# Optimization experiments

Hardware: AMD Instinct MI355X
Metric: run time of the kernel (lower is better)

## Reference

```python
import jax, jax.numpy as jnp
import numpy as np

TEMPERATURE = 0.07


def setup_inputs() -> dict:
    key = jax.random.key(0)
    k1, k2 = jax.random.split(key)
    B, D = 8192, 1024
    emb1 = jax.random.normal(k1, (B, D), dtype=jnp.float32)
    emb2 = jax.random.normal(k2, (B, D), dtype=jnp.float32)
    return {"emb1": emb1, "emb2": emb2}


def reference(emb1, emb2):
    B = emb1.shape[0]
    # [B, B] similarity logits scaled by temperature
    logits = jnp.matmul(emb1, emb2.T) / TEMPERATURE
    # SigLIP-style contrastive loss: diagonal entries are positives,
    # off-diagonal entries are negatives.
    # positive: -logsigmoid(logits) on diag; negative: -logsigmoid(-logits) off-diag
    pos = -jax.nn.log_sigmoid(jnp.diagonal(logits))            # [B]
    neg = -jax.nn.log_sigmoid(-logits)                          # [B, B]
    # negative_mask zeroes the diagonal -> subtract diagonal contribution
    neg_sum = neg.sum() - jnp.sum(jnp.diagonal(neg))
    loss = (pos.sum() + neg_sum) / B
    return loss
```

## Files before the change

kernel.cpp:

```cpp
#include <hip/hip_runtime.h>


#define B_DIM 8192
#define K_DIM 1024
#define BT 128
#define BKB 128
#define NT (K_DIM / BKB)
#define BRICK 16384
#define PANEL_BYTES (NT * BRICK)
#define BUFSZ 32768

typedef int i32x4 __attribute__((ext_vector_type(4)));
typedef int i32x8 __attribute__((ext_vector_type(8)));
typedef float f32x4 __attribute__((ext_vector_type(4)));

__device__ __forceinline__ void brick_store(const float* __restrict__ in,
                                            unsigned char* __restrict__ out,
                                            float scale, int i) {
  const int o = i * 16;
  const int b = o >> 14;
  const int p = b >> 3, t = b & 7;
  const int w = o & (BRICK - 1);
  const int fb = w >> 11;
  const int h = (w >> 10) & 1;
  const int kch = (w >> 8) & 3;
  const int lr = (w >> 4) & 15;
  const int row = p * 128 + fb * 16 + lr;
  const int kb = t * 128 + kch * 32 + h * 16;
  const float4* src = (const float4*)(in + (size_t)row * K_DIM + kb);
  float4 v0 = src[0], v1 = src[1], v2 = src[2], v3 = src[3];
  unsigned w0 = 0, w1 = 0, w2 = 0, w3 = 0;
  w0 = __builtin_amdgcn_cvt_pk_fp8_f32(v0.x * scale, v0.y * scale, w0, 0);
  w0 = __builtin_amdgcn_cvt_pk_fp8_f32(v0.z * scale, v0.w * scale, w0, 1);
  w1 = __builtin_amdgcn_cvt_pk_fp8_f32(v1.x * scale, v1.y * scale, w1, 0);
  w1 = __builtin_amdgcn_cvt_pk_fp8_f32(v1.z * scale, v1.w * scale, w1, 1);
  w2 = __builtin_amdgcn_cvt_pk_fp8_f32(v2.x * scale, v2.y * scale, w2, 0);
  w2 = __builtin_amdgcn_cvt_pk_fp8_f32(v2.z * scale, v2.w * scale, w2, 1);
  w3 = __builtin_amdgcn_cvt_pk_fp8_f32(v3.x * scale, v3.y * scale, w3, 0);
  w3 = __builtin_amdgcn_cvt_pk_fp8_f32(v3.z * scale, v3.w * scale, w3, 1);
  *(uint4*)(out + o) = make_uint4(w0, w1, w2, w3);
}

__global__ __launch_bounds__(256) void cvt_fused(
    const float* __restrict__ e1, const float* __restrict__ e2,
    unsigned char* __restrict__ A8, unsigned char* __restrict__ B8,
    int nbA, float scaleA) {
  const int blk = blockIdx.x;
  if (blk < nbA)
    brick_store(e1, A8, scaleA, blk * 256 + threadIdx.x);
  else
    brick_store(e2, B8, 1.0f, (blk - nbA) * 256 + threadIdx.x);
}

template <bool DIAG>
__device__ __forceinline__ float softplus_sum(const f32x4 (&acc)[4][4],
                                              int rbase, int cbase) {
  float lin = 0.f, cor = 0.f;
#pragma unroll
  for (int m = 0; m < 4; ++m) {
#pragma unroll
    for (int n = 0; n < 4; ++n) {
#pragma unroll
      for (int r = 0; r < 4; ++r) {
        float x = acc[m][n][r];
        if (DIAG) {
          int row = rbase + m * 16 + r;
          int col = cbase + n * 16;
          if (row == col) x = -x;
        }
        lin += fmaxf(x, 0.f);
        cor += __logf(1.f + __expf(-fabsf(x)));
      }
    }
  }
  return lin + cor;
}

#define STAGEA(SB, Q, TI)                                                     \
  __builtin_amdgcn_global_load_lds(                                           \
      (const __attribute__((address_space(1))) void*)(const void*)(           \
          srcA + (TI) * BRICK + (Q) * 1024),                                  \
      (__attribute__((address_space(3))) void*)(void*)(                       \
          lds + (SB) + dA + (Q) * 1024),                                      \
      16, 0, 0)
#define STAGEB(SB, Q, TI)                                                     \
  __builtin_amdgcn_global_load_lds(                                           \
      (const __attribute__((address_space(1))) void*)(const void*)(           \
          srcB + (TI) * BRICK + (Q) * 1024),                                  \
      (__attribute__((address_space(3))) void*)(void*)(                       \
          lds + (SB) + dB + (Q) * 1024),                                      \
      16, 0, 0)

#define LDA(OUT, RB, M)                                                       \
  {                                                                           \
    const unsigned char* _b = ldsL + ((RB) + ((wr * 4 + (M)) << 11));         \
    i32x4 _lo = *(const i32x4*)(_b);                                          \
    i32x4 _hi = *(const i32x4*)(_b + 1024);                                   \
    OUT = __builtin_shufflevector(_lo, _hi, 0, 1, 2, 3, 4, 5, 6, 7);          \
  }
#define LDB(OUT, RB, N)                                                       \
  {                                                                           \
    const unsigned char* _b = ldsL + ((RB) + 16384 + ((wc * 4 + (N)) << 11)); \
    i32x4 _lo = *(const i32x4*)(_b);                                          \
    i32x4 _hi = *(const i32x4*)(_b + 1024);                                   \
    OUT = __builtin_shufflevector(_lo, _hi, 0, 1, 2, 3, 4, 5, 6, 7);          \
  }

#define MFMA(AF, BF, M, N)                                                    \
  acc[M][N] = __builtin_amdgcn_mfma_scale_f32_16x16x128_f8f6f4(               \
      AF, BF, acc[M][N], 0, 0, 0, 127, 0, 127)

__global__ __launch_bounds__(256, 2) void siglip_gemm(
    const unsigned char* __restrict__ A8,
    const unsigned char* __restrict__ B8,
    float* __restrict__ partials) {
  __shared__ unsigned char lds[2 * BUFSZ];
  __shared__ float wsum[4];

  const int tid = threadIdx.x;
  const int wave = tid >> 6;
  const int lane = tid & 63;
  const int wr = wave >> 1;
  const int wc = wave & 1;
  const int brow = blockIdx.y;
  const int bcol = blockIdx.x;

  f32x4 acc[4][4];
#pragma unroll
  for (int m = 0; m < 4; ++m)
#pragma unroll
    for (int n = 0; n < 4; ++n) acc[m][n] = f32x4{0.f, 0.f, 0.f, 0.f};

  const unsigned char* srcA =
      A8 + (size_t)brow * PANEL_BYTES + wave * 4096 + (lane << 4);
  const unsigned char* srcB =
      B8 + (size_t)bcol * PANEL_BYTES + wave * 4096 + (lane << 4);
  const int dA = wave * 4096;
  const int dB = 16384 + wave * 4096;
  const unsigned char* ldsL = lds + (lane << 4);

  STAGEA(0, 0, 0); STAGEA(0, 1, 0); STAGEA(0, 2, 0); STAGEA(0, 3, 0);
  STAGEB(0, 0, 0); STAGEB(0, 1, 0); STAGEB(0, 2, 0); STAGEB(0, 3, 0);
  asm volatile("s_waitcnt vmcnt(0)" ::: "memory");
  __builtin_amdgcn_s_barrier();
  __builtin_amdgcn_sched_barrier(0);

#pragma unroll
  for (int T = 0; T < NT; ++T) {
    const int rb = (T & 1) * BUFSZ;
    const int sb = rb ^ BUFSZ;

    if (T < NT - 1) {
      STAGEA(sb, 0, T + 1); STAGEA(sb, 1, T + 1);
      STAGEA(sb, 2, T + 1); STAGEA(sb, 3, T + 1);
      STAGEB(sb, 0, T + 1); STAGEB(sb, 1, T + 1);
      STAGEB(sb, 2, T + 1); STAGEB(sb, 3, T + 1);
    }

    i32x8 a0, a1, a2, a3, b0, b1, b2, b3;
    LDA(a0, rb, 0); LDB(b0, rb, 0); LDB(b1, rb, 1); LDB(b2, rb, 2);
    LDB(b3, rb, 3);
    LDA(a1, rb, 1); LDA(a2, rb, 2); LDA(a3, rb, 3);

    __builtin_amdgcn_s_setprio(1);
    MFMA(a0, b0, 0, 0); MFMA(a0, b1, 0, 1); MFMA(a0, b2, 0, 2); MFMA(a0, b3, 0, 3);
    MFMA(a1, b0, 1, 0); MFMA(a1, b1, 1, 1); MFMA(a1, b2, 1, 2); MFMA(a1, b3, 1, 3);
    MFMA(a2, b0, 2, 0); MFMA(a2, b1, 2, 1); MFMA(a2, b2, 2, 2); MFMA(a2, b3, 2, 3);
    MFMA(a3, b0, 3, 0); MFMA(a3, b1, 3, 1); MFMA(a3, b2, 3, 2); MFMA(a3, b3, 3, 3);
    __builtin_amdgcn_s_setprio(0);

    if (T < NT - 1) {
      asm volatile("s_waitcnt vmcnt(0)" ::: "memory");
      __builtin_amdgcn_s_barrier();
      __builtin_amdgcn_sched_barrier(0);
    }
  }

  const int rbase = brow * BT + wr * 64 + (lane >> 4) * 4;
  const int cbase = bcol * BT + wc * 64 + (lane & 15);
  float lsum;
  if (brow == bcol)
    lsum = softplus_sum<true>(acc, rbase, cbase);
  else
    lsum = softplus_sum<false>(acc, rbase, cbase);

#pragma unroll
  for (int off = 32; off > 0; off >>= 1) lsum += __shfl_down(lsum, off);
  __syncthreads();
  if (lane == 0) wsum[wave] = lsum;
  __syncthreads();
  if (tid == 0)
    partials[blockIdx.y * gridDim.x + blockIdx.x] =
        wsum[0] + wsum[1] + wsum[2] + wsum[3];
}

__global__ void reduce_kernel(const float* __restrict__ partials, int n,
                              float* __restrict__ out) {
  __shared__ float s[256];
  float v = 0.f;
  for (int i = threadIdx.x; i < n; i += 256) v += partials[i];
  s[threadIdx.x] = v;
  __syncthreads();
  for (int off = 128; off > 0; off >>= 1) {
    if ((int)threadIdx.x < off) s[threadIdx.x] += s[threadIdx.x + off];
    __syncthreads();
  }
  if (threadIdx.x == 0) out[0] = s[0] / (float)B_DIM;
}

extern "C" void kernel_launch(void* const* d_in, const int* in_sizes, int n_in,
                              void* d_out, int out_size, void* d_ws, size_t ws_size,
                              hipStream_t stream) {
  const float* emb1 = (const float*)d_in[0];
  const float* emb2 = (const float*)d_in[1];

  unsigned char* A8 = (unsigned char*)d_ws;
  unsigned char* B8 = A8 + (size_t)B_DIM * K_DIM;
  float* partials = (float*)(B8 + (size_t)B_DIM * K_DIM);

  const float INV_T = 1.0f / 0.07f;
  const int nbA = (B_DIM * K_DIM / 16) / 256;
  cvt_fused<<<2 * nbA, 256, 0, stream>>>(emb1, emb2, A8, B8, nbA, INV_T);

  dim3 grid(B_DIM / BT, B_DIM / BT);
  siglip_gemm<<<grid, 256, 0, stream>>>(A8, B8, partials);

  const int nparts = (B_DIM / BT) * (B_DIM / BT);
  reduce_kernel<<<1, 256, 0, stream>>>(partials, nparts, (float*)d_out);
}
```

Baseline: 115.6 us.

## Use 256x128 tiles with 8 waves and a triple-buffered LDS pipeline

```diff
diff --git a/kernel.cpp b/kernel.cpp
--- a/kernel.cpp
+++ b/kernel.cpp
@@ -3,12 +3,11 @@
 
 #define B_DIM 8192
 #define K_DIM 1024
-#define BT 128
 #define BKB 128
 #define NT (K_DIM / BKB)
 #define BRICK 16384
 #define PANEL_BYTES (NT * BRICK)
-#define BUFSZ 32768
+#define BUFSZ 49152
 
 typedef int i32x4 __attribute__((ext_vector_type(4)));
 typedef int i32x8 __attribute__((ext_vector_type(8)));
@@ -90,32 +89,67 @@
       (__attribute__((address_space(3))) void*)(void*)(                       \
           lds + (SB) + dB + (Q) * 1024),                                      \
       16, 0, 0)
+#define STAGE6(SB, TI)                                                        \
+  STAGEA(SB, 0, TI); STAGEA(SB, 1, TI); STAGEA(SB, 2, TI); STAGEA(SB, 3, TI); \
+  STAGEB(SB, 0, TI); STAGEB(SB, 1, TI)
 
 #define LDA(OUT, RB, M)                                                       \
   {                                                                           \
-    const unsigned char* _b = ldsL + ((RB) + ((wr * 4 + (M)) << 11));         \
+    const unsigned char* _b =                                                 \
+        ldsL + ((RB) + ((wr >> 1) * 16384) + (((wr & 1) * 4 + (M)) << 11));   \
     i32x4 _lo = *(const i32x4*)(_b);                                          \
     i32x4 _hi = *(const i32x4*)(_b + 1024);                                   \
     OUT = __builtin_shufflevector(_lo, _hi, 0, 1, 2, 3, 4, 5, 6, 7);          \
   }
 #define LDB(OUT, RB, N)                                                       \
   {                                                                           \
-    const unsigned char* _b = ldsL + ((RB) + 16384 + ((wc * 4 + (N)) << 11)); \
+    const unsigned char* _b = ldsL + ((RB) + 32768 + ((wc * 4 + (N)) << 11)); \
     i32x4 _lo = *(const i32x4*)(_b);                                          \
     i32x4 _hi = *(const i32x4*)(_b + 1024);                                   \
     OUT = __builtin_shufflevector(_lo, _hi, 0, 1, 2, 3, 4, 5, 6, 7);          \
   }
-
-#define MFMA(AF, BF, M, N)                                                    \
+#define READS(RB, FA, FB)                                                     \
+  LDA(FA[0], RB, 0); LDB(FB[0], RB, 0); LDB(FB[1], RB, 1);                    \
+  LDB(FB[2], RB, 2); LDB(FB[3], RB, 3);                                       \
+  LDA(FA[1], RB, 1); LDA(FA[2], RB, 2); LDA(FA[3], RB, 3)
+
+#define MFMA1(AF, BF, M, N)                                                   \
   acc[M][N] = __builtin_amdgcn_mfma_scale_f32_16x16x128_f8f6f4(               \
       AF, BF, acc[M][N], 0, 0, 0, 127, 0, 127)
-
-__global__ __launch_bounds__(256, 2) void siglip_gemm(
+#define MFMAS(FA, FB)                                                         \
+  __builtin_amdgcn_s_setprio(1);                                              \
+  MFMA1(FA[0], FB[0], 0, 0); MFMA1(FA[0], FB[1], 0, 1);                       \
+  MFMA1(FA[0], FB[2], 0, 2); MFMA1(FA[0], FB[3], 0, 3);                       \
+  MFMA1(FA[1], FB[0], 1, 0); MFMA1(FA[1], FB[1], 1, 1);                       \
+  MFMA1(FA[1], FB[2], 1, 2); MFMA1(FA[1], FB[3], 1, 3);                       \
+  MFMA1(FA[2], FB[0], 2, 0); MFMA1(FA[2], FB[1], 2, 1);                       \
+  MFMA1(FA[2], FB[2], 2, 2); MFMA1(FA[2], FB[3], 2, 3);                       \
+  MFMA1(FA[3], FB[0], 3, 0); MFMA1(FA[3], FB[1], 3, 1);                       \
+  MFMA1(FA[3], FB[2], 3, 2); MFMA1(FA[3], FB[3], 3, 3);                       \
+  __builtin_amdgcn_s_setprio(0)
+
+#define ITER(T, FAc, FBc, FAn, FBn)                                           \
+  {                                                                           \
+    if ((T) < NT - 2) { STAGE6((((T) + 2) % 3) * BUFSZ, (T) + 2); }           \
+    if ((T) < NT - 2) {                                                       \
+      asm volatile("s_waitcnt vmcnt(6)" ::: "memory");                        \
+    } else if ((T) == NT - 2) {                                               \
+      asm volatile("s_waitcnt vmcnt(0)" ::: "memory");                        \
+    }                                                                         \
+    if ((T) < NT - 1) {                                                       \
+      __builtin_amdgcn_s_barrier();                                           \
+      __builtin_amdgcn_sched_barrier(0);                                      \
+      READS((((T) + 1) % 3) * BUFSZ, FAn, FBn);                               \
+    }                                                                         \
+    MFMAS(FAc, FBc);                                                          \
+  }
+
+__global__ __launch_bounds__(512, 1) void siglip_gemm(
     const unsigned char* __restrict__ A8,
     const unsigned char* __restrict__ B8,
     float* __restrict__ partials) {
-  __shared__ unsigned char lds[2 * BUFSZ];
-  __shared__ float wsum[4];
+  __shared__ unsigned char lds[3 * BUFSZ];
+  __shared__ float wsum[8];
 
   const int tid = threadIdx.x;
   const int wave = tid >> 6;
@@ -131,55 +165,37 @@
 #pragma unroll
     for (int n = 0; n < 4; ++n) acc[m][n] = f32x4{0.f, 0.f, 0.f, 0.f};
 
-  const unsigned char* srcA =
-      A8 + (size_t)brow * PANEL_BYTES + wave * 4096 + (lane << 4);
+  const unsigned char* srcA = A8 +
+      (size_t)(2 * brow + (wave >> 2)) * PANEL_BYTES + (wave & 3) * 4096 +
+      (lane << 4);
   const unsigned char* srcB =
-      B8 + (size_t)bcol * PANEL_BYTES + wave * 4096 + (lane << 4);
-  const int dA = wave * 4096;
-  const int dB = 16384 + wave * 4096;
+      B8 + (size_t)bcol * PANEL_BYTES + wave * 2048 + (lane << 4);
+  const int dA = (wave >> 2) * 16384 + (wave & 3) * 4096;
+  const int dB = 32768 + wave * 2048;
   const unsigned char* ldsL = lds + (lane << 4);
 
-  STAGEA(0, 0, 0); STAGEA(0, 1, 0); STAGEA(0, 2, 0); STAGEA(0, 3, 0);
-  STAGEB(0, 0, 0); STAGEB(0, 1, 0); STAGEB(0, 2, 0); STAGEB(0, 3, 0);
-  asm volatile("s_waitcnt vmcnt(0)" ::: "memory");
+  i32x8 fa0[4], fb0[4], fa1[4], fb1[4];
+
+  STAGE6(0, 0);
+  STAGE6(BUFSZ, 1);
+  asm volatile("s_waitcnt vmcnt(6)" ::: "memory");
   __builtin_amdgcn_s_barrier();
   __builtin_amdgcn_sched_barrier(0);
-
-#pragma unroll
-  for (int T = 0; T < NT; ++T) {
-    const int rb = (T & 1) * BUFSZ;
-    const int sb = rb ^ BUFSZ;
-
-    if (T < NT - 1) {
-      STAGEA(sb, 0, T + 1); STAGEA(sb, 1, T + 1);
-      STAGEA(sb, 2, T + 1); STAGEA(sb, 3, T + 1);
-      STAGEB(sb, 0, T + 1); STAGEB(sb, 1, T + 1);
-      STAGEB(sb, 2, T + 1); STAGEB(sb, 3, T + 1);
-    }
-
-    i32x8 a0, a1, a2, a3, b0, b1, b2, b3;
-    LDA(a0, rb, 0); LDB(b0, rb, 0); LDB(b1, rb, 1); LDB(b2, rb, 2);
-    LDB(b3, rb, 3);
-    LDA(a1, rb, 1); LDA(a2, rb, 2); LDA(a3, rb, 3);
-
-    __builtin_amdgcn_s_setprio(1);
-    MFMA(a0, b0, 0, 0); MFMA(a0, b1, 0, 1); MFMA(a0, b2, 0, 2); MFMA(a0, b3, 0, 3);
-    MFMA(a1, b0, 1, 0); MFMA(a1, b1, 1, 1); MFMA(a1, b2, 1, 2); MFMA(a1, b3, 1, 3);
-    MFMA(a2, b0, 2, 0); MFMA(a2, b1, 2, 1); MFMA(a2, b2, 2, 2); MFMA(a2, b3, 2, 3);
-    MFMA(a3, b0, 3, 0); MFMA(a3, b1, 3, 1); MFMA(a3, b2, 3, 2); MFMA(a3, b3, 3, 3);
-    __builtin_amdgcn_s_setprio(0);
-
-    if (T < NT - 1) {
-      asm volatile("s_waitcnt vmcnt(0)" ::: "memory");
-      __builtin_amdgcn_s_barrier();
-      __builtin_amdgcn_sched_barrier(0);
-    }
-  }
-
-  const int rbase = brow * BT + wr * 64 + (lane >> 4) * 4;
-  const int cbase = bcol * BT + wc * 64 + (lane & 15);
+  READS(0, fa0, fb0);
+
+  ITER(0, fa0, fb0, fa1, fb1)
+  ITER(1, fa1, fb1, fa0, fb0)
+  ITER(2, fa0, fb0, fa1, fb1)
+  ITER(3, fa1, fb1, fa0, fb0)
+  ITER(4, fa0, fb0, fa1, fb1)
+  ITER(5, fa1, fb1, fa0, fb0)
+  ITER(6, fa0, fb0, fa1, fb1)
+  ITER(7, fa1, fb1, fa0, fb0)
+
+  const int rbase = brow * 256 + wr * 64 + (lane >> 4) * 4;
+  const int cbase = bcol * 128 + wc * 64 + (lane & 15);
   float lsum;
-  if (brow == bcol)
+  if ((bcol >> 1) == brow)
     lsum = softplus_sum<true>(acc, rbase, cbase);
   else
     lsum = softplus_sum<false>(acc, rbase, cbase);
@@ -189,9 +205,12 @@
   __syncthreads();
   if (lane == 0) wsum[wave] = lsum;
   __syncthreads();
-  if (tid == 0)
-    partials[blockIdx.y * gridDim.x + blockIdx.x] =
-        wsum[0] + wsum[1] + wsum[2] + wsum[3];
+  if (tid == 0) {
+    float s = 0.f;
+#pragma unroll
+    for (int w = 0; w < 8; ++w) s += wsum[w];
+    partials[blockIdx.y * gridDim.x + blockIdx.x] = s;
+  }
 }
 
 __global__ void reduce_kernel(const float* __restrict__ partials, int n,
@@ -222,9 +241,9 @@
   const int nbA = (B_DIM * K_DIM / 16) / 256;
   cvt_fused<<<2 * nbA, 256, 0, stream>>>(emb1, emb2, A8, B8, nbA, INV_T);
 
-  dim3 grid(B_DIM / BT, B_DIM / BT);
-  siglip_gemm<<<grid, 256, 0, stream>>>(A8, B8, partials);
-
-  const int nparts = (B_DIM / BT) * (B_DIM / BT);
+  dim3 grid(B_DIM / 128, B_DIM / 256);
+  siglip_gemm<<<grid, 512, 0, stream>>>(A8, B8, partials);
+
+  const int nparts = (B_DIM / 256) * (B_DIM / 128);
   reduce_kernel<<<1, 256, 0, stream>>>(partials, nparts, (float*)d_out);
 }
```

Result: slower. 120.3 us (+4.1%).

## Single-buffer LDS staging to raise occupancy to five blocks per CU

Applied to the files above, without the earlier changes.

```diff
diff --git a/kernel.cpp b/kernel.cpp
--- a/kernel.cpp
+++ b/kernel.cpp
@@ -8,7 +8,6 @@
 #define NT (K_DIM / BKB)
 #define BRICK 16384
 #define PANEL_BYTES (NT * BRICK)
-#define BUFSZ 32768
 
 typedef int i32x4 __attribute__((ext_vector_type(4)));
 typedef int i32x8 __attribute__((ext_vector_type(8)));
@@ -76,31 +75,34 @@
   return lin + cor;
 }
 
-#define STAGEA(SB, Q, TI)                                                     \
+#define STAGEA(Q, TI)                                                         \
   __builtin_amdgcn_global_load_lds(                                           \
       (const __attribute__((address_space(1))) void*)(const void*)(           \
           srcA + (TI) * BRICK + (Q) * 1024),                                  \
       (__attribute__((address_space(3))) void*)(void*)(                       \
-          lds + (SB) + dA + (Q) * 1024),                                      \
+          lds + dA + (Q) * 1024),                                             \
       16, 0, 0)
-#define STAGEB(SB, Q, TI)                                                     \
+#define STAGEB(Q, TI)                                                         \
   __builtin_amdgcn_global_load_lds(                                           \
       (const __attribute__((address_space(1))) void*)(const void*)(           \
           srcB + (TI) * BRICK + (Q) * 1024),                                  \
       (__attribute__((address_space(3))) void*)(void*)(                       \
-          lds + (SB) + dB + (Q) * 1024),                                      \
+          lds + dB + (Q) * 1024),                                             \
       16, 0, 0)
-
-#define LDA(OUT, RB, M)                                                       \
+#define STAGE8(TI)                                                            \
+  STAGEA(0, TI); STAGEA(1, TI); STAGEA(2, TI); STAGEA(3, TI);                 \
+  STAGEB(0, TI); STAGEB(1, TI); STAGEB(2, TI); STAGEB(3, TI)
+
+#define LDA(OUT, M)                                                           \
   {                                                                           \
-    const unsigned char* _b = ldsL + ((RB) + ((wr * 4 + (M)) << 11));         \
+    const unsigned char* _b = ldsL + ((wr * 4 + (M)) << 11);                  \
     i32x4 _lo = *(const i32x4*)(_b);                                          \
     i32x4 _hi = *(const i32x4*)(_b + 1024);                                   \
     OUT = __builtin_shufflevector(_lo, _hi, 0, 1, 2, 3, 4, 5, 6, 7);          \
   }
-#define LDB(OUT, RB, N)                                                       \
+#define LDB(OUT, N)                                                           \
   {                                                                           \
-    const unsigned char* _b = ldsL + ((RB) + 16384 + ((wc * 4 + (N)) << 11)); \
+    const unsigned char* _b = ldsL + (16384 + ((wc * 4 + (N)) << 11));        \
     i32x4 _lo = *(const i32x4*)(_b);                                          \
     i32x4 _hi = *(const i32x4*)(_b + 1024);                                   \
     OUT = __builtin_shufflevector(_lo, _hi, 0, 1, 2, 3, 4, 5, 6, 7);          \
@@ -110,12 +112,11 @@
   acc[M][N] = __builtin_amdgcn_mfma_scale_f32_16x16x128_f8f6f4(               \
       AF, BF, acc[M][N], 0, 0, 0, 127, 0, 127)
 
-__global__ __launch_bounds__(256, 2) void siglip_gemm(
+__global__ __launch_bounds__(256, 5) void siglip_gemm(
     const unsigned char* __restrict__ A8,
     const unsigned char* __restrict__ B8,
     float* __restrict__ partials) {
-  __shared__ unsigned char lds[2 * BUFSZ];
-  __shared__ float wsum[4];
+  __shared__ unsigned char lds[32768];
 
   const int tid = threadIdx.x;
   const int wave = tid >> 6;
@@ -139,28 +140,22 @@
   const int dB = 16384 + wave * 4096;
   const unsigned char* ldsL = lds + (lane << 4);
 
-  STAGEA(0, 0, 0); STAGEA(0, 1, 0); STAGEA(0, 2, 0); STAGEA(0, 3, 0);
-  STAGEB(0, 0, 0); STAGEB(0, 1, 0); STAGEB(0, 2, 0); STAGEB(0, 3, 0);
-  asm volatile("s_waitcnt vmcnt(0)" ::: "memory");
-  __builtin_amdgcn_s_barrier();
-  __builtin_amdgcn_sched_barrier(0);
+  STAGE8(0);
 
 #pragma unroll
   for (int T = 0; T < NT; ++T) {
-    const int rb = (T & 1) * BUFSZ;
-    const int sb = rb ^ BUFSZ;
+    __syncthreads();
+
+    i32x8 a0, a1, a2, a3, b0, b1, b2, b3;
+    LDA(a0, 0); LDB(b0, 0); LDB(b1, 1); LDB(b2, 2); LDB(b3, 3);
+    LDA(a1, 1); LDA(a2, 2); LDA(a3, 3);
+
+    __syncthreads();
 
     if (T < NT - 1) {
-      STAGEA(sb, 0, T + 1); STAGEA(sb, 1, T + 1);
-      STAGEA(sb, 2, T + 1); STAGEA(sb, 3, T + 1);
-      STAGEB(sb, 0, T + 1); STAGEB(sb, 1, T + 1);
-      STAGEB(sb, 2, T + 1); STAGEB(sb, 3, T + 1);
+      STAGE8(T + 1);
+      __builtin_amdgcn_sched_barrier(0);
     }
-
-    i32x8 a0, a1, a2, a3, b0, b1, b2, b3;
-    LDA(a0, rb, 0); LDB(b0, rb, 0); LDB(b1, rb, 1); LDB(b2, rb, 2);
-    LDB(b3, rb, 3);
-    LDA(a1, rb, 1); LDA(a2, rb, 2); LDA(a3, rb, 3);
 
     __builtin_amdgcn_s_setprio(1);
     MFMA(a0, b0, 0, 0); MFMA(a0, b1, 0, 1); MFMA(a0, b2, 0, 2); MFMA(a0, b3, 0, 3);
@@ -168,12 +163,6 @@
     MFMA(a2, b0, 2, 0); MFMA(a2, b1, 2, 1); MFMA(a2, b2, 2, 2); MFMA(a2, b3, 2, 3);
     MFMA(a3, b0, 3, 0); MFMA(a3, b1, 3, 1); MFMA(a3, b2, 3, 2); MFMA(a3, b3, 3, 3);
     __builtin_amdgcn_s_setprio(0);
-
-    if (T < NT - 1) {
-      asm volatile("s_waitcnt vmcnt(0)" ::: "memory");
-      __builtin_amdgcn_s_barrier();
-      __builtin_amdgcn_sched_barrier(0);
-    }
   }
 
   const int rbase = brow * BT + wr * 64 + (lane >> 4) * 4;
@@ -186,6 +175,8 @@
 
 #pragma unroll
   for (int off = 32; off > 0; off >>= 1) lsum += __shfl_down(lsum, off);
+
+  float* wsum = (float*)lds;
   __syncthreads();
   if (lane == 0) wsum[wave] = lsum;
   __syncthreads();
```

Result: slower. 449.8 us (+289.3%).
